# Kernel optimization log

Hardware: AMD Instinct MI355X
Metric: run time of the kernel (lower is better)

The kernel has to match this reference:

```python
import jax, jax.numpy as jnp
import numpy as np

ENC_DIM = 512
QUERY_DIM = 1024
ATTN_DIM = 128
CONV_CH = 32
KERNEL = 31
B, T = 64, 2048


def setup_inputs() -> dict:
    key = jax.random.key(0)
    ks = jax.random.split(key, 9)
    s = 0.02
    encoder_outputs = jax.random.normal(ks[0], (B, T, ENC_DIM), dtype=jnp.float32)
    decoder_hidden = jax.random.normal(ks[1], (B, QUERY_DIM), dtype=jnp.float32)
    prev_attention = jax.random.uniform(ks[2], (B, T), dtype=jnp.float32)
    prev_attention = prev_attention / jnp.sum(prev_attention, axis=1, keepdims=True)
    Wq = jax.random.normal(ks[3], (QUERY_DIM, ATTN_DIM), dtype=jnp.float32) * s
    Wk = jax.random.normal(ks[4], (ENC_DIM, ATTN_DIM), dtype=jnp.float32) * s
    conv_w = jax.random.normal(ks[5], (CONV_CH, 1, KERNEL), dtype=jnp.float32) * s  # OIH
    conv_b = jax.random.normal(ks[6], (CONV_CH,), dtype=jnp.float32) * s
    Wloc = jax.random.normal(ks[7], (CONV_CH, ATTN_DIM), dtype=jnp.float32) * s
    v = jax.random.normal(ks[8], (ATTN_DIM,), dtype=jnp.float32) * s
    return {"encoder_outputs": encoder_outputs, "decoder_hidden": decoder_hidden,
            "prev_attention": prev_attention, "Wq": Wq, "Wk": Wk,
            "conv_w": conv_w, "conv_b": conv_b, "Wloc": Wloc, "v": v}


def reference(encoder_outputs, decoder_hidden, prev_attention, Wq, Wk, conv_w, conv_b, Wloc, v):
    # query: [B, 1, A]
    query = (decoder_hidden @ Wq)[:, None, :]
    # keys: [B, T, A]
    keys = jnp.einsum('bte,ea->bta', encoder_outputs, Wk)
    # location conv: prev_attention [B, T] -> [B, 1, T] -> [B, C, T], SAME padding
    pad = (KERNEL - 1) // 2
    loc = jax.lax.conv_general_dilated(
        prev_attention[:, None, :], conv_w,
        window_strides=(1,), padding=[(pad, pad)],
        dimension_numbers=('NCH', 'OIH', 'NCH'))
    loc = loc + conv_b[None, :, None]
    # [B, T, C] -> [B, T, A]
    location_term = jnp.einsum('bct,ca->bta', loc, Wloc)
    energy = jnp.einsum('bta,a->bt', jnp.tanh(keys + query + location_term), v)
    return jax.nn.softmax(energy, axis=1)
```

## Files before the change

### kernel.cpp

```cpp
#include <hip/hip_runtime.h>
#include <hip/hip_bf16.h>

#define B_  64
#define T_  2048
#define E_  512
#define Q_  1024
#define A_  128
#define C_  32
#define KW_ 31

using bf16x8 = __attribute__((ext_vector_type(8))) short;
using f32x4  = __attribute__((ext_vector_type(4))) float;

__device__ __forceinline__ short f2bf(float f) {
  union { float f; unsigned u; } x; x.f = f;
  unsigned r = x.u + 0x7fffu + ((x.u >> 16) & 1u);
  return (short)(r >> 16);
}

__device__ __forceinline__ bf16x8 pack8(float4 a, float4 b) {
  union { bf16x8 v; __hip_bfloat162 h[4]; } u;
  u.h[0] = __float22bfloat162_rn(make_float2(a.x, a.y));
  u.h[1] = __float22bfloat162_rn(make_float2(a.z, a.w));
  u.h[2] = __float22bfloat162_rn(make_float2(b.x, b.y));
  u.h[3] = __float22bfloat162_rn(make_float2(b.z, b.w));
  return u.v;
}

__device__ __forceinline__ float fast_tanh(float x) {
  float e2 = __expf(2.f * x);
  return 1.f - 2.f * __builtin_amdgcn_rcpf(e2 + 1.f);
}

__global__ __launch_bounds__(256) void prep_kernel(
    const float* __restrict__ dh, const float* __restrict__ Wq,
    const float* __restrict__ conv_b, const float* __restrict__ Wloc,
    const float* __restrict__ Wk,
    unsigned short* __restrict__ wkf, unsigned short* __restrict__ wlocf,
    float* __restrict__ q2p)
{
  int blk = blockIdx.x;
  int tid = threadIdx.x;
  if (blk < 512) {
    __shared__ float part[128];
    int b = blk >> 3, kq = blk & 7;
    int a = tid & 127, kh = tid >> 7;
    const float* dhr = dh + b * Q_ + kq * 128 + kh * 64;
    const float* wq  = Wq + (size_t)(kq * 128 + kh * 64) * A_ + a;
    float s = 0.f;
    #pragma unroll 8
    for (int k = 0; k < 64; ++k) s += dhr[k] * wq[(size_t)k * A_];
    if (kh) part[a] = s;
    __syncthreads();
    if (!kh) {
      s += part[a];
      if (kq == 0) {
        float t = 0.f;
        #pragma unroll 8
        for (int c = 0; c < C_; ++c) t += conv_b[c] * Wloc[c * A_ + a];
        s += t;
      }
      q2p[(kq * B_ + b) * A_ + a] = s;
    }
  } else if (blk < 544) {
    int wave = tid >> 6, lane = tid & 63;
    int g = (blk - 512) * 4 + wave;
    int ks = g >> 3, nt = g & 7;
    int lg = lane >> 4, lr = lane & 15;
    bf16x8 o;
    #pragma unroll
    for (int j = 0; j < 8; ++j)
      o[j] = f2bf(Wk[(ks * 32 + lg * 8 + j) * A_ + nt * 16 + lr]);
    *(bf16x8*)(wkf + ((size_t)g * 64 + lane) * 8) = o;
  } else {
    int wave = tid >> 6, lane = tid & 63;
    int g = (blk - 544) * 4 + wave;
    int lg = lane >> 4, lr = lane & 15;
    bf16x8 o;
    #pragma unroll
    for (int j = 0; j < 8; ++j)
      o[j] = f2bf(Wloc[(lg * 8 + j) * A_ + g * 16 + lr]);
    *(bf16x8*)(wlocf + ((size_t)g * 64 + lane) * 8) = o;
  }
}

__global__ __launch_bounds__(256) void energy_kernel(
    const float* __restrict__ enc, const float* __restrict__ prev,
    const float* __restrict__ conv_w,
    const unsigned short* __restrict__ wkf, const unsigned short* __restrict__ wlocf,
    const float* __restrict__ q2p, const float* __restrict__ vvec,
    float* __restrict__ energy)
{
  __shared__ float sprev[160];
  __shared__ float scw[KW_][C_];
  __shared__ unsigned short slocb[128][C_];
  int tid = threadIdx.x;
  int m0 = blockIdx.x * 128;
  int b  = m0 >> 11, t0 = m0 & (T_ - 1);

  for (int i = tid; i < 158; i += 256) {
    int t = t0 - 15 + i;
    sprev[i] = (t >= 0 && t < T_) ? prev[b * T_ + t] : 0.f;
  }
  for (int i = tid; i < KW_ * C_; i += 256) {
    int j = i >> 5, c = i & 31;
    scw[j][c] = conv_w[c * KW_ + j];
  }
  __syncthreads();
  {
    int tl = tid >> 1, ch0 = (tid & 1) * 16;
    float acc[16];
    #pragma unroll
    for (int c = 0; c < 16; ++c) acc[c] = 0.f;
    for (int j = 0; j < KW_; ++j) {
      float p = sprev[tl + j];
      #pragma unroll
      for (int c = 0; c < 16; ++c) acc[c] += p * scw[j][ch0 + c];
    }
    unsigned int* dstp = (unsigned int*)&slocb[tl][ch0];
    #pragma unroll
    for (int c = 0; c < 16; c += 2)
      dstp[c >> 1] = ((unsigned int)(unsigned short)f2bf(acc[c + 1]) << 16)
                   | (unsigned short)f2bf(acc[c]);
  }
  __syncthreads();

  int wave = tid >> 6, lane = tid & 63;
  int lg = lane >> 4, lr = lane & 15;
  int wm = m0 + wave * 32;

  const float* encRow0 = enc + (size_t)(wm + lr) * E_ + lg * 8;
  const float* encRow1 = encRow0 + 16 * E_;

  f32x4 acc0[8], acc1[8];
  #pragma unroll
  for (int i = 0; i < 8; ++i) { acc0[i] = (f32x4){0,0,0,0}; acc1[i] = (f32x4){0,0,0,0}; }

  const unsigned short* wkl = wkf + (size_t)lane * 8;
  #pragma unroll 2
  for (int ks = 0; ks < 16; ++ks) {
    float4 a0 = *(const float4*)(encRow0 + ks * 32);
    float4 a1 = *(const float4*)(encRow0 + ks * 32 + 4);
    float4 a2 = *(const float4*)(encRow1 + ks * 32);
    float4 a3 = *(const float4*)(encRow1 + ks * 32 + 4);
    bf16x8 af0 = pack8(a0, a1);
    bf16x8 af1 = pack8(a2, a3);
    #pragma unroll
    for (int nt = 0; nt < 8; ++nt) {
      bf16x8 bf = *(const bf16x8*)(wkl + (size_t)(ks * 8 + nt) * 64 * 8);
      acc0[nt] = __builtin_amdgcn_mfma_f32_16x16x32_bf16(af0, bf, acc0[nt], 0, 0, 0);
      acc1[nt] = __builtin_amdgcn_mfma_f32_16x16x32_bf16(af1, bf, acc1[nt], 0, 0, 0);
    }
  }
  {
    int lrow = wave * 32 + lr;
    bf16x8 af0 = *(const bf16x8*)&slocb[lrow][lg * 8];
    bf16x8 af1 = *(const bf16x8*)&slocb[lrow + 16][lg * 8];
    #pragma unroll
    for (int nt = 0; nt < 8; ++nt) {
      bf16x8 bf = *(const bf16x8*)(wlocf + ((size_t)nt * 64 + lane) * 8);
      acc0[nt] = __builtin_amdgcn_mfma_f32_16x16x32_bf16(af0, bf, acc0[nt], 0, 0, 0);
      acc1[nt] = __builtin_amdgcn_mfma_f32_16x16x32_bf16(af1, bf, acc1[nt], 0, 0, 0);
    }
  }
  float qv[8], vv[8];
  #pragma unroll
  for (int nt = 0; nt < 8; ++nt) {
    int n = nt * 16 + lr;
    float s = 0.f;
    #pragma unroll
    for (int p = 0; p < 8; ++p) s += q2p[(p * B_ + b) * A_ + n];
    qv[nt] = s;
    vv[nt] = vvec[n];
  }
  #pragma unroll
  for (int f = 0; f < 2; ++f) {
    f32x4* acc = f ? acc1 : acc0;
    float p0 = 0, p1 = 0, p2 = 0, p3 = 0;
    #pragma unroll
    for (int nt = 0; nt < 8; ++nt) {
      p0 += fast_tanh(acc[nt][0] + qv[nt]) * vv[nt];
      p1 += fast_tanh(acc[nt][1] + qv[nt]) * vv[nt];
      p2 += fast_tanh(acc[nt][2] + qv[nt]) * vv[nt];
      p3 += fast_tanh(acc[nt][3] + qv[nt]) * vv[nt];
    }
    #pragma unroll
    for (int off = 1; off < 16; off <<= 1) {
      p0 += __shfl_xor(p0, off, 64);
      p1 += __shfl_xor(p1, off, 64);
      p2 += __shfl_xor(p2, off, 64);
      p3 += __shfl_xor(p3, off, 64);
    }
    if (lr == 0)
      *(float4*)(energy + wm + f * 16 + lg * 4) = make_float4(p0, p1, p2, p3);
  }
}

__global__ __launch_bounds__(256) void softmax_kernel(float* __restrict__ out)
{
  int bb = blockIdx.x;
  int tid = threadIdx.x;
  float* row = out + (size_t)bb * T_;
  float vals[8];
  float m = -1e30f;
  #pragma unroll
  for (int i = 0; i < 8; ++i) { vals[i] = row[tid + i * 256]; m = fmaxf(m, vals[i]); }
  #pragma unroll
  for (int off = 1; off < 64; off <<= 1) m = fmaxf(m, __shfl_xor(m, off, 64));
  __shared__ float sm[4], ss[4];
  int wv = tid >> 6, ln = tid & 63;
  if (ln == 0) sm[wv] = m;
  __syncthreads();
  m = fmaxf(fmaxf(sm[0], sm[1]), fmaxf(sm[2], sm[3]));
  float s = 0.f;
  #pragma unroll
  for (int i = 0; i < 8; ++i) { vals[i] = __expf(vals[i] - m); s += vals[i]; }
  #pragma unroll
  for (int off = 1; off < 64; off <<= 1) s += __shfl_xor(s, off, 64);
  if (ln == 0) ss[wv] = s;
  __syncthreads();
  s = ss[0] + ss[1] + ss[2] + ss[3];
  float inv = 1.f / s;
  #pragma unroll
  for (int i = 0; i < 8; ++i) row[tid + i * 256] = vals[i] * inv;
}

extern "C" void kernel_launch(void* const* d_in, const int* in_sizes, int n_in,
                              void* d_out, int out_size, void* d_ws, size_t ws_size,
                              hipStream_t stream)
{
  const float* enc   = (const float*)d_in[0];
  const float* dh    = (const float*)d_in[1];
  const float* prev  = (const float*)d_in[2];
  const float* Wq    = (const float*)d_in[3];
  const float* Wk    = (const float*)d_in[4];
  const float* convw = (const float*)d_in[5];
  const float* convb = (const float*)d_in[6];
  const float* Wloc  = (const float*)d_in[7];
  const float* v     = (const float*)d_in[8];
  float* out = (float*)d_out;

  char* w = (char*)d_ws;
  unsigned short* wkf   = (unsigned short*)w;
  unsigned short* wlocf = (unsigned short*)(w + 131072);
  float*          q2p   = (float*)(w + 139264);

  hipLaunchKernelGGL(prep_kernel, dim3(546), dim3(256), 0, stream,
                     dh, Wq, convb, Wloc, Wk, wkf, wlocf, q2p);
  hipLaunchKernelGGL(energy_kernel, dim3(1024), dim3(256), 0, stream,
                     enc, prev, convw, wkf, wlocf, q2p, v, out);
  hipLaunchKernelGGL(softmax_kernel, dim3(64), dim3(256), 0, stream, out);
}
```

Baseline: 78.85 us.

## Stage Wk tiles into LDS with double-buffered async loads and fuse softmax exp

```diff
diff --git a/kernel.cpp b/kernel.cpp
--- a/kernel.cpp
+++ b/kernel.cpp
@@ -30,6 +30,12 @@
 __device__ __forceinline__ float fast_tanh(float x) {
   float e2 = __expf(2.f * x);
   return 1.f - 2.f * __builtin_amdgcn_rcpf(e2 + 1.f);
+}
+
+__device__ __forceinline__ void gload16(const void* g, void* l) {
+  __builtin_amdgcn_global_load_lds(
+      (const __attribute__((address_space(1))) unsigned int*)g,
+      (__attribute__((address_space(3))) unsigned int*)l, 16, 0, 0);
 }
 
 __global__ __launch_bounds__(256) void prep_kernel(
@@ -84,16 +90,20 @@
   }
 }
 
-__global__ __launch_bounds__(256) void energy_kernel(
+__global__ __launch_bounds__(256, 4) void energy_kernel(
     const float* __restrict__ enc, const float* __restrict__ prev,
     const float* __restrict__ conv_w,
-    const unsigned short* __restrict__ wkf, const unsigned short* __restrict__ wlocf,
+    const unsigned short* __restrict__ wkfall,
     const float* __restrict__ q2p, const float* __restrict__ vvec,
-    float* __restrict__ energy)
+    float* __restrict__ outexp, float* __restrict__ psum)
 {
+  __shared__ unsigned short sB0[4096];
+  __shared__ unsigned short sB1[4096];
   __shared__ float sprev[160];
   __shared__ float scw[KW_][C_];
   __shared__ unsigned short slocb[128][C_];
+  __shared__ float swsum[4];
+
   int tid = threadIdx.x;
   int m0 = blockIdx.x * 128;
   int b  = m0 >> 11, t0 = m0 & (T_ - 1);
@@ -132,37 +142,84 @@
   const float* encRow0 = enc + (size_t)(wm + lr) * E_ + lg * 8;
   const float* encRow1 = encRow0 + 16 * E_;
 
+  #define STAGE(slice, buf) do {                                              \
+    const unsigned short* s_ = wkfall + (size_t)(slice) * 4096 + wave * 512 + lane * 8; \
+    gload16(s_,        &buf[wave * 512]);                                     \
+    gload16(s_ + 2048, &buf[(4 + wave) * 512]);                               \
+  } while (0)
+
   f32x4 acc0[8], acc1[8];
   #pragma unroll
   for (int i = 0; i < 8; ++i) { acc0[i] = (f32x4){0,0,0,0}; acc1[i] = (f32x4){0,0,0,0}; }
 
-  const unsigned short* wkl = wkf + (size_t)lane * 8;
-  #pragma unroll 2
-  for (int ks = 0; ks < 16; ++ks) {
-    float4 a0 = *(const float4*)(encRow0 + ks * 32);
-    float4 a1 = *(const float4*)(encRow0 + ks * 32 + 4);
-    float4 a2 = *(const float4*)(encRow1 + ks * 32);
-    float4 a3 = *(const float4*)(encRow1 + ks * 32 + 4);
-    bf16x8 af0 = pack8(a0, a1);
-    bf16x8 af1 = pack8(a2, a3);
-    #pragma unroll
-    for (int nt = 0; nt < 8; ++nt) {
-      bf16x8 bf = *(const bf16x8*)(wkl + (size_t)(ks * 8 + nt) * 64 * 8);
-      acc0[nt] = __builtin_amdgcn_mfma_f32_16x16x32_bf16(af0, bf, acc0[nt], 0, 0, 0);
-      acc1[nt] = __builtin_amdgcn_mfma_f32_16x16x32_bf16(af1, bf, acc1[nt], 0, 0, 0);
-    }
-  }
+  float4 aA0, aA1, aA2, aA3, aB0, aB1, aB2, aB3;
+
+  STAGE(0, sB0);
+  __builtin_amdgcn_sched_barrier(0);
+  aA0 = *(const float4*)(encRow0);     aA1 = *(const float4*)(encRow0 + 4);
+  aA2 = *(const float4*)(encRow1);     aA3 = *(const float4*)(encRow1 + 4);
+  asm volatile("s_waitcnt vmcnt(4)" ::: "memory");
+  __builtin_amdgcn_sched_barrier(0);
+  __builtin_amdgcn_s_barrier();
+
+  #pragma unroll 1
+  for (int i = 0; i < 8; ++i) {
+    STAGE(2 * i + 1, sB1);
+    __builtin_amdgcn_sched_barrier(0);
+    {
+      const float* r0 = encRow0 + (2 * i + 1) * 32;
+      const float* r1 = encRow1 + (2 * i + 1) * 32;
+      aB0 = *(const float4*)(r0); aB1 = *(const float4*)(r0 + 4);
+      aB2 = *(const float4*)(r1); aB3 = *(const float4*)(r1 + 4);
+    }
+    {
+      bf16x8 af0 = pack8(aA0, aA1), af1 = pack8(aA2, aA3);
+      #pragma unroll
+      for (int nt = 0; nt < 8; ++nt) {
+        bf16x8 bfr = *(const bf16x8*)&sB0[nt * 512 + lane * 8];
+        acc0[nt] = __builtin_amdgcn_mfma_f32_16x16x32_bf16(af0, bfr, acc0[nt], 0, 0, 0);
+        acc1[nt] = __builtin_amdgcn_mfma_f32_16x16x32_bf16(af1, bfr, acc1[nt], 0, 0, 0);
+      }
+    }
+    asm volatile("s_waitcnt vmcnt(4) lgkmcnt(0)" ::: "memory");
+    __builtin_amdgcn_sched_barrier(0);
+    __builtin_amdgcn_s_barrier();
+
+    STAGE(2 * i + 2, sB0);
+    __builtin_amdgcn_sched_barrier(0);
+    if (i < 7) {
+      const float* r0 = encRow0 + (2 * i + 2) * 32;
+      const float* r1 = encRow1 + (2 * i + 2) * 32;
+      aA0 = *(const float4*)(r0); aA1 = *(const float4*)(r0 + 4);
+      aA2 = *(const float4*)(r1); aA3 = *(const float4*)(r1 + 4);
+    }
+    {
+      bf16x8 af0 = pack8(aB0, aB1), af1 = pack8(aB2, aB3);
+      #pragma unroll
+      for (int nt = 0; nt < 8; ++nt) {
+        bf16x8 bfr = *(const bf16x8*)&sB1[nt * 512 + lane * 8];
+        acc0[nt] = __builtin_amdgcn_mfma_f32_16x16x32_bf16(af0, bfr, acc0[nt], 0, 0, 0);
+        acc1[nt] = __builtin_amdgcn_mfma_f32_16x16x32_bf16(af1, bfr, acc1[nt], 0, 0, 0);
+      }
+    }
+    if (i < 7) { asm volatile("s_waitcnt vmcnt(4) lgkmcnt(0)" ::: "memory"); }
+    else       { asm volatile("s_waitcnt vmcnt(0) lgkmcnt(0)" ::: "memory"); }
+    __builtin_amdgcn_sched_barrier(0);
+    __builtin_amdgcn_s_barrier();
+  }
+
   {
     int lrow = wave * 32 + lr;
     bf16x8 af0 = *(const bf16x8*)&slocb[lrow][lg * 8];
     bf16x8 af1 = *(const bf16x8*)&slocb[lrow + 16][lg * 8];
     #pragma unroll
     for (int nt = 0; nt < 8; ++nt) {
-      bf16x8 bf = *(const bf16x8*)(wlocf + ((size_t)nt * 64 + lane) * 8);
-      acc0[nt] = __builtin_amdgcn_mfma_f32_16x16x32_bf16(af0, bf, acc0[nt], 0, 0, 0);
-      acc1[nt] = __builtin_amdgcn_mfma_f32_16x16x32_bf16(af1, bf, acc1[nt], 0, 0, 0);
-    }
-  }
+      bf16x8 bfr = *(const bf16x8*)&sB0[nt * 512 + lane * 8];
+      acc0[nt] = __builtin_amdgcn_mfma_f32_16x16x32_bf16(af0, bfr, acc0[nt], 0, 0, 0);
+      acc1[nt] = __builtin_amdgcn_mfma_f32_16x16x32_bf16(af1, bfr, acc1[nt], 0, 0, 0);
+    }
+  }
+
   float qv[8], vv[8];
   #pragma unroll
   for (int nt = 0; nt < 8; ++nt) {
@@ -173,6 +230,7 @@
     qv[nt] = s;
     vv[nt] = vvec[n];
   }
+  float ssum = 0.f;
   #pragma unroll
   for (int f = 0; f < 2; ++f) {
     f32x4* acc = f ? acc1 : acc0;
@@ -191,38 +249,34 @@
       p2 += __shfl_xor(p2, off, 64);
       p3 += __shfl_xor(p3, off, 64);
     }
+    float e0 = __expf(p0), e1 = __expf(p1), e2 = __expf(p2), e3 = __expf(p3);
+    ssum += (e0 + e1) + (e2 + e3);
     if (lr == 0)
-      *(float4*)(energy + wm + f * 16 + lg * 4) = make_float4(p0, p1, p2, p3);
-  }
-}
-
-__global__ __launch_bounds__(256) void softmax_kernel(float* __restrict__ out)
+      *(float4*)(outexp + wm + f * 16 + lg * 4) = make_float4(e0, e1, e2, e3);
+  }
+  ssum += __shfl_xor(ssum, 16, 64);
+  ssum += __shfl_xor(ssum, 32, 64);
+  if (lane == 0) swsum[wave] = ssum;
+  __syncthreads();
+  if (tid == 0)
+    psum[b * 16 + (blockIdx.x & 15)] = (swsum[0] + swsum[1]) + (swsum[2] + swsum[3]);
+}
+
+__global__ __launch_bounds__(256) void norm_kernel(float* __restrict__ out,
+                                                   const float* __restrict__ psum)
 {
-  int bb = blockIdx.x;
-  int tid = threadIdx.x;
-  float* row = out + (size_t)bb * T_;
-  float vals[8];
-  float m = -1e30f;
-  #pragma unroll
-  for (int i = 0; i < 8; ++i) { vals[i] = row[tid + i * 256]; m = fmaxf(m, vals[i]); }
-  #pragma unroll
-  for (int off = 1; off < 64; off <<= 1) m = fmaxf(m, __shfl_xor(m, off, 64));
-  __shared__ float sm[4], ss[4];
-  int wv = tid >> 6, ln = tid & 63;
-  if (ln == 0) sm[wv] = m;
-  __syncthreads();
-  m = fmaxf(fmaxf(sm[0], sm[1]), fmaxf(sm[2], sm[3]));
+  int b = blockIdx.x, tid = threadIdx.x;
   float s = 0.f;
   #pragma unroll
-  for (int i = 0; i < 8; ++i) { vals[i] = __expf(vals[i] - m); s += vals[i]; }
-  #pragma unroll
-  for (int off = 1; off < 64; off <<= 1) s += __shfl_xor(s, off, 64);
-  if (ln == 0) ss[wv] = s;
-  __syncthreads();
-  s = ss[0] + ss[1] + ss[2] + ss[3];
+  for (int p = 0; p < 16; ++p) s += psum[b * 16 + p];
   float inv = 1.f / s;
-  #pragma unroll
-  for (int i = 0; i < 8; ++i) row[tid + i * 256] = vals[i] * inv;
+  float4* row = (float4*)(out + (size_t)b * T_);
+  #pragma unroll
+  for (int j = 0; j < 2; ++j) {
+    float4 x = row[tid + j * 256];
+    x.x *= inv; x.y *= inv; x.z *= inv; x.w *= inv;
+    row[tid + j * 256] = x;
+  }
 }
 
 extern "C" void kernel_launch(void* const* d_in, const int* in_sizes, int n_in,
@@ -244,10 +298,11 @@
   unsigned short* wkf   = (unsigned short*)w;
   unsigned short* wlocf = (unsigned short*)(w + 131072);
   float*          q2p   = (float*)(w + 139264);
+  float*          psum  = (float*)(w + 401408);
 
   hipLaunchKernelGGL(prep_kernel, dim3(546), dim3(256), 0, stream,
                      dh, Wq, convb, Wloc, Wk, wkf, wlocf, q2p);
   hipLaunchKernelGGL(energy_kernel, dim3(1024), dim3(256), 0, stream,
-                     enc, prev, convw, wkf, wlocf, q2p, v, out);
-  hipLaunchKernelGGL(softmax_kernel, dim3(64), dim3(256), 0, stream, out);
-}
+                     enc, prev, convw, wkf, q2p, v, out, psum);
+  hipLaunchKernelGGL(norm_kernel, dim3(64), dim3(256), 0, stream, out, psum);
+}
```

Measured after the change: 72.73 us. -7.8%, faster.
